# Optimization experiments

Measured on AMD Instinct MI355X. Metric: run time of the kernel, lower is better.

## Reference

```python
import jax, jax.numpy as jnp
import numpy as np

B, T, C = 8, 2048, 1024
HS = 64           # head_size
H = C // HS       # n_head = 16
LORA_R = 32       # per-branch lora rank (A is C x 32*5)
TD_R = 64         # time-decay lora rank


def setup_inputs() -> dict:
    key = jax.random.key(0)
    ks = jax.random.split(key, 20)
    inp = {
        "x": jax.random.normal(ks[0], (B, T, C), jnp.float32),
        "miu_x": jax.random.uniform(ks[1], (1, 1, C), jnp.float32),
        "lambda_": jax.random.uniform(ks[2], (5, 1, 1, C), jnp.float32),
        "A_lora": jax.random.normal(ks[3], (C, LORA_R * 5), jnp.float32) * 0.01,
        "B_lora": jax.random.normal(ks[4], (5, LORA_R, C), jnp.float32) * 0.01,
        "td_miu": -6.0 + 5.0 * jax.random.uniform(ks[5], (1, 1, C), jnp.float32),
        "td_A": jax.random.normal(ks[6], (C, TD_R), jnp.float32) * 0.01,
        "td_B": jax.random.normal(ks[7], (TD_R, C), jnp.float32) * 0.01,
        "u": jax.random.normal(ks[8], (H, HS), jnp.float32) * 0.1,
        "Wr": jax.random.normal(ks[9], (C, C), jnp.float32) * 0.02,
        "Wk": jax.random.normal(ks[10], (C, C), jnp.float32) * 0.02,
        "Wv": jax.random.normal(ks[11], (C, C), jnp.float32) * 0.02,
        "Wg": jax.random.normal(ks[12], (C, C), jnp.float32) * 0.02,
        "Wo": jax.random.normal(ks[13], (C, C), jnp.float32) * 0.02,
        "gn_gamma": jnp.ones((C,), jnp.float32),
        "gn_beta": jnp.zeros((C,), jnp.float32),
    }
    return inp


def _wkv6(r, k, v, w, u):
    """RWKV-6 selective-decay linear attention scan.
    r,k,v,w: (b, h, t, n); u: (h, n). Returns y: (b, h, t, n).
    State update: S = diag(exp(-exp(w_t))) S + k_t^T v_t;
    output: y_t = r_t @ (S + diag-free bonus u*k_t^T v_t)."""
    n = r.shape[-1]
    decay = jnp.exp(-jnp.exp(w))  # (b,h,t,n)

    def per_head(rt, kt, vt, dt, uh):  # (t,n) each, uh (n,)
        def step(S, inp):
            ri, ki, vi, di = inp
            kv = ki[:, None] * vi[None, :]          # (n,n)
            y = ri @ (S + uh[:, None] * kv)          # (n,)
            S = di[:, None] * S + kv
            return S, y
        S0 = jnp.zeros((n, n), rt.dtype)
        _, ys = jax.lax.scan(step, S0, (rt, kt, vt, dt))
        return ys  # (t,n)

    f = jax.vmap(per_head, in_axes=(0, 0, 0, 0, 0))       # heads
    f = jax.vmap(f, in_axes=(0, 0, 0, 0, None))           # batch
    return f(r, k, v, decay, u)


def reference(x, miu_x, lambda_, A_lora, B_lora, td_miu, td_A, td_B, u,
              Wr, Wk, Wv, Wg, Wo, gn_gamma, gn_beta):
    b, t, c = x.shape
    h, n = u.shape

    # time_shift: ZeroPad2d((0,0,1,-1)) -> previous token, zeros at t=0
    x_last = jnp.pad(x, ((0, 0), (1, 0), (0, 0)))[:, :t]
    dxa = x_last - x

    # ddlerp: lerp with static miu_x, then data-dependent LoRA mixing coeffs
    xm = x + dxa * miu_x  # (b,t,c)
    lora_h = jnp.tanh(xm @ A_lora).reshape(b, t, 5, -1)        # (b,t,5,32)
    miu = lambda_ + jnp.einsum('btfi,fic->fbtc', lora_h, B_lora)  # (5,b,t,c)
    xx = x[None] + dxa[None] * miu                             # (5,b,t,c)
    w_in, k_in, v_in, r_in, g_in = xx

    k = k_in @ Wk.T
    v = v_in @ Wv.T
    r = r_in @ Wr.T
    g = jax.nn.silu(g_in @ Wg.T)
    w = td_miu + jnp.tanh(w_in @ td_A) @ td_B  # (b,t,c)

    def to_heads(z):
        return z.reshape(b, t, h, n).transpose(0, 2, 1, 3)  # (b,h,t,n)

    y = _wkv6(to_heads(r), to_heads(k), to_heads(v), to_heads(w), u)
    y = y.transpose(0, 2, 1, 3)  # (b,t,h,n)

    # GroupNorm(n_head groups over C) per token, eps = 1e-5 * n_head
    eps = 1e-5 * h
    mean = y.mean(-1, keepdims=True)
    var = y.var(-1, keepdims=True)
    yn = (y - mean) * jax.lax.rsqrt(var + eps)
    yn = yn * gn_gamma.reshape(h, n) + gn_beta.reshape(h, n)
    yn = yn.reshape(b, t, c)

    return (yn * g) @ Wo.T
```

## Files before the change

### kernel.cpp

```cpp
#include <hip/hip_runtime.h>
#include <hip/hip_bf16.h>
#include <cstdint>

typedef __bf16 bf16_t;
typedef __bf16 bf16x8 __attribute__((ext_vector_type(8)));
typedef float f32x4 __attribute__((ext_vector_type(4)));

#define BB 8
#define TT 2048
#define TC 512
#define TCLOG 9
#define NCHUNK 4
#define MCH (BB*TC)
#define CCH 1024
#define HH 16
#define HSZ 64
#define LR5 160
#define LRP 192
#define TDR 64
#define TDK 128
#define TSUB 64
#define NSC (TC/TSUB)
#define BBHH (BB*HH)
#define LDP 72

#define BM 128
#define BN 128
#define BKK 64

enum { EPI_NONE = 0, EPI_SILU = 1, EPI_TANH = 2, EPI_XX = 3, EPI_WBIAS = 4 };

__device__ __forceinline__ void gload16(const bf16_t* g, bf16_t* l) {
    __builtin_amdgcn_global_load_lds(
        (__attribute__((address_space(1))) void*)(g),
        (__attribute__((address_space(3))) void*)(l), 16, 0, 0);
}

__global__ __launch_bounds__(256) void f2b_kernel(const float* __restrict__ in,
        bf16_t* __restrict__ out, int n) {
    int i = blockIdx.x * 256 + threadIdx.x;
    if (i < n) out[i] = (bf16_t)in[i];
}

__global__ __launch_bounds__(256) void transb_pad(const float* __restrict__ in,
        bf16_t* __restrict__ out, int R, int Cc, int Cp) {
    int i = blockIdx.x * 256 + threadIdx.x;
    if (i >= Cp * R) return;
    int row = i / R, col = i - row * R;
    out[i] = (row < Cc) ? (bf16_t)in[(size_t)col * Cc + row] : (bf16_t)0.f;
}

__global__ __launch_bounds__(256) void bbig_pad(const float* __restrict__ B_lora,
        bf16_t* __restrict__ Bbig) {
    int i = blockIdx.x * 256 + threadIdx.x;
    if (i >= 5 * CCH * LRP) return;
    int row = i / LRP, col = i - row * LRP;
    int f = row >> 10, c = row & (CCH - 1);
    int lo = f * 32;
    float v = 0.f;
    if (col >= lo && col < lo + 32)
        v = B_lora[(size_t)(lo + (col - lo)) * CCH + c];
    Bbig[i] = (bf16_t)v;
}

__global__ __launch_bounds__(256) void tdb2_kernel(const float* __restrict__ td_B,
        bf16_t* __restrict__ tdB2) {
    int i = blockIdx.x * 256 + threadIdx.x;
    if (i >= CCH * TDR) return;
    int n = i >> 6, k = i & 63;
    float f = td_B[(size_t)k * CCH + n];
    bf16_t hi = (bf16_t)f;
    bf16_t lo = (bf16_t)(f - (float)hi);
    tdB2[(size_t)n * TDK + k] = hi;
    tdB2[(size_t)n * TDK + TDR + k] = lo;
}

__global__ __launch_bounds__(256) void xm_kernel(const float* __restrict__ x,
        const float* __restrict__ miu_x, bf16_t* __restrict__ xm, int cOff) {
    long long i = (long long)blockIdx.x * 256 + threadIdx.x;
    int ch = (int)(i & (CCH - 1));
    int btl = (int)(i >> 10);
    int b = btl >> TCLOG, tau = btl & (TC - 1);
    int t = cOff + tau;
    size_t gi = ((size_t)b * TT + t) * CCH + ch;
    float xv = x[gi];
    float xp = (t > 0) ? x[gi - CCH] : 0.f;
    xm[i] = (bf16_t)(xv + (xp - xv) * miu_x[ch]);
}

struct GJob {
    const bf16_t* A;
    const bf16_t* Bw;
    void* C;
    int N;
    int nbmax;
    int K;
    int ldc;
    int epi;
    int outf32;
    int cmap;
    int dup;
};
struct GJobs { GJob j[5]; };

__global__ __launch_bounds__(256) void gemm_jobs(GJobs jobs,
        const float* __restrict__ x, const float* __restrict__ lam,
        const float* __restrict__ tdmiu, bf16_t* __restrict__ xx5, int cOff) {
    const GJob jb = jobs.j[blockIdx.z];
    const int n0 = blockIdx.y * BN;
    if (n0 >= jb.nbmax) return;
    const int m0 = blockIdx.x * BM;
    const int K = jb.K;
    __shared__ __align__(16) bf16_t As[BM * BKK];
    __shared__ __align__(16) bf16_t Bs[BN * BKK];
    const int tid = threadIdx.x;
    const int w = tid >> 6, lane = tid & 63;
    const int wm = (w >> 1) * 64, wn = (w & 1) * 64;
    const int lrow = lane & 15;
    const int kq = (lane >> 4) * 8;
    const int srow = tid >> 3;
    const int sc8 = (tid & 7) * 8;
    const bf16_t* Ab = jb.A + (size_t)m0 * K;
    const bf16_t* Bb = jb.Bw + (size_t)n0 * K;
    f32x4 acc[4][4] = {};
    for (int k0 = 0; k0 < K; k0 += BKK) {
        __syncthreads();
        #pragma unroll
        for (int p = 0; p < 4; ++p) {
            int r = srow + p * 32;
            gload16(Ab + (size_t)r * K + k0 + sc8, &As[(tid + p * 256) * 8]);
            gload16(Bb + (size_t)r * K + k0 + sc8, &Bs[(tid + p * 256) * 8]);
        }
        __syncthreads();
        #pragma unroll
        for (int kk = 0; kk < BKK; kk += 32) {
            bf16x8 af[4], bfr[4];
            #pragma unroll
            for (int mt = 0; mt < 4; ++mt)
                af[mt] = *(const bf16x8*)(&As[(wm + mt * 16 + lrow) * BKK + kk + kq]);
            #pragma unroll
            for (int nt = 0; nt < 4; ++nt)
                bfr[nt] = *(const bf16x8*)(&Bs[(wn + nt * 16 + lrow) * BKK + kk + kq]);
            #pragma unroll
            for (int mt = 0; mt < 4; ++mt)
                #pragma unroll
                for (int nt = 0; nt < 4; ++nt)
                    acc[mt][nt] = __builtin_amdgcn_mfma_f32_16x16x32_bf16(
                        af[mt], bfr[nt], acc[mt][nt], 0, 0, 0);
        }
    }
    const int rbase = (lane >> 4) * 4;
    const int col = lane & 15;
    if (jb.epi == EPI_XX) {
        #pragma unroll
        for (int mt = 0; mt < 4; ++mt)
            #pragma unroll
            for (int nt = 0; nt < 4; ++nt) {
                int n = n0 + wn + nt * 16 + col;
                int f = n >> 10, cch = n & (CCH - 1);
                #pragma unroll
                for (int rg = 0; rg < 4; ++rg) {
                    int m = m0 + wm + mt * 16 + rbase + rg;
                    int b = m >> TCLOG, tau = m & (TC - 1);
                    int t = cOff + tau;
                    size_t gi = ((size_t)b * TT + t) * CCH + cch;
                    float xv = x[gi];
                    float xp = (t > 0) ? x[gi - CCH] : 0.f;
                    float miu = lam[f * CCH + cch] + acc[mt][nt][rg];
                    xx5[(size_t)(f * MCH + m) * CCH + cch] =
                        (bf16_t)(xv + (xp - xv) * miu);
                }
            }
        return;
    }
    #pragma unroll
    for (int mt = 0; mt < 4; ++mt) {
        #pragma unroll
        for (int nt = 0; nt < 4; ++nt) {
            int n = n0 + wn + nt * 16 + col;
            if (n >= jb.N) continue;
            #pragma unroll
            for (int rg = 0; rg < 4; ++rg) {
                int m = m0 + wm + mt * 16 + rbase + rg;
                size_t mg = jb.cmap ? ((size_t)(m >> TCLOG) * TT + cOff + (m & (TC - 1)))
                                    : (size_t)m;
                float vv = acc[mt][nt][rg];
                if (jb.epi == EPI_SILU) vv = vv / (1.f + expf(-vv));
                else if (jb.epi == EPI_TANH) vv = tanhf(vv);
                else if (jb.epi == EPI_WBIAS) vv += tdmiu[n];
                if (jb.outf32) {
                    ((float*)jb.C)[mg * jb.ldc + n] = vv;
                } else {
                    bf16_t hv = (bf16_t)vv;
                    ((bf16_t*)jb.C)[mg * jb.ldc + n] = hv;
                    if (jb.dup) ((bf16_t*)jb.C)[mg * jb.ldc + n + TDR] = hv;
                }
            }
        }
    }
}

__global__ __launch_bounds__(64) void wkv_prepsg(const bf16_t* __restrict__ ry,
        const bf16_t* __restrict__ k, const float* __restrict__ w,
        const bf16_t* __restrict__ v, const float* __restrict__ u,
        bf16_t* __restrict__ rrT, bf16_t* __restrict__ ktT,
        float* __restrict__ PL, float* __restrict__ bvec,
        float* __restrict__ Sloc) {
    const int bh = blockIdx.x, sc = blockIdx.y;
    const int b = bh >> 4, h = bh & 15;
    const int j = threadIdx.x;
    const size_t base = ((size_t)b * TC + sc * TSUB) * CCH + h * HSZ + j;
    const size_t tile = ((size_t)bh * NSC + sc) * (TSUB * HSZ);
    const size_t vb = (size_t)bh * NSC + sc;
    __shared__ __align__(16) bf16_t ksT[HSZ * LDP];
    __shared__ __align__(16) bf16_t vtT[HSZ * LDP];
    __shared__ float pls[HSZ];
    const float uj = u[h * HSZ + j];
    float pex = 1.f;
    for (int t = 0; t < TSUB; ++t) {
        size_t idx = base + (size_t)t * CCH;
        float rv = (float)ry[idx], kv = (float)k[idx], wv = w[idx];
        bf16_t vv = v[idx];
        float d = expf(-expf(wv));
        rrT[tile + t * HSZ + j] = (bf16_t)(rv * pex);
        float pinc = pex * d;
        bf16_t ktv = (bf16_t)(kv / pinc);
        ktT[tile + t * HSZ + j] = ktv;
        ksT[j * LDP + t] = ktv;
        vtT[j * LDP + t] = vv;
        float bu = rv * uj * kv;
        #pragma unroll
        for (int off = 1; off < 64; off <<= 1) bu += __shfl_xor(bu, off);
        if (j == 0) bvec[vb * TSUB + t] = bu;
        pex = pinc;
    }
    PL[vb * HSZ + j] = pex;
    pls[j] = pex;
    __syncthreads();
    const int lrow = j & 15, kq = (j >> 4) * 8;
    f32x4 acc[4][4] = {};
    #pragma unroll
    for (int kk = 0; kk < TSUB; kk += 32) {
        bf16x8 af[4], bfr[4];
        #pragma unroll
        for (int mt = 0; mt < 4; ++mt)
            af[mt] = *(const bf16x8*)(&ksT[(mt * 16 + lrow) * LDP + kk + kq]);
        #pragma unroll
        for (int nt = 0; nt < 4; ++nt)
            bfr[nt] = *(const bf16x8*)(&vtT[(nt * 16 + lrow) * LDP + kk + kq]);
        #pragma unroll
        for (int mt = 0; mt < 4; ++mt)
            #pragma unroll
            for (int nt = 0; nt < 4; ++nt)
                acc[mt][nt] = __builtin_amdgcn_mfma_f32_16x16x32_bf16(
                    af[mt], bfr[nt], acc[mt][nt], 0, 0, 0);
    }
    const int rbase = (j >> 4) * 4, col = j & 15;
    #pragma unroll
    for (int mt = 0; mt < 4; ++mt)
        #pragma unroll
        for (int nt = 0; nt < 4; ++nt)
            #pragma unroll
            for (int rg = 0; rg < 4; ++rg) {
                int i = mt * 16 + rbase + rg, n = nt * 16 + col;
                Sloc[tile + i * HSZ + n] = pls[i] * acc[mt][nt][rg];
            }
}

__global__ __launch_bounds__(64) void wkv_combine(const float* __restrict__ Sloc,
        const float* __restrict__ PL, float* __restrict__ S0st,
        float* state, int cOuter) {
    const int bh = blockIdx.x;
    const int j = threadIdx.x;
    float* st = state + (size_t)bh * HSZ * HSZ;
    float S[HSZ];
    if (cOuter > 0) {
        #pragma unroll
        for (int i = 0; i < HSZ; ++i) S[i] = st[i * HSZ + j];
    } else {
        #pragma unroll
        for (int i = 0; i < HSZ; ++i) S[i] = 0.f;
    }
    __shared__ float pls[HSZ];
    for (int sc = 0; sc < NSC; ++sc) {
        const size_t so = ((size_t)bh * NSC + sc) * (HSZ * HSZ);
        pls[j] = PL[((size_t)bh * NSC + sc) * HSZ + j];
        __syncthreads();
        #pragma unroll
        for (int i = 0; i < HSZ; ++i) {
            S0st[so + i * HSZ + j] = S[i];
            S[i] = pls[i] * S[i] + Sloc[so + i * HSZ + j];
        }
        __syncthreads();
    }
    #pragma unroll
    for (int i = 0; i < HSZ; ++i) st[i * HSZ + j] = S[i];
}

__global__ __launch_bounds__(64) void wkv_y(bf16_t* __restrict__ ry,
        const bf16_t* __restrict__ rrT, const bf16_t* __restrict__ ktT,
        const bf16_t* __restrict__ v, const float* __restrict__ S0st,
        const float* __restrict__ bvec) {
    const int bh = blockIdx.x, sc = blockIdx.y;
    const int b = bh >> 4, h = bh & 15;
    const int j = threadIdx.x;
    const size_t tile = ((size_t)bh * NSC + sc) * (TSUB * HSZ);
    const size_t basev = ((size_t)b * TC + sc * TSUB) * CCH + h * HSZ;
    __shared__ __align__(16) bf16_t vtT[HSZ * LDP];
    __shared__ __align__(16) bf16_t s0T[HSZ * LDP];
    __shared__ __align__(16) bf16_t am[TSUB * LDP];
    __shared__ float bl[TSUB];
    for (int s = 0; s < TSUB; ++s)
        vtT[j * LDP + s] = v[basev + (size_t)s * CCH + j];
    for (int i = 0; i < HSZ; ++i)
        s0T[j * LDP + i] = (bf16_t)S0st[tile + i * HSZ + j];
    bl[j] = bvec[((size_t)bh * NSC + sc) * TSUB + j];
    __syncthreads();
    const bf16_t* rrt = rrT + tile;
    const bf16_t* ktt = ktT + tile;
    const int lane = j;
    const int lrow = lane & 15, kq = (lane >> 4) * 8;
    const int rbase = (lane >> 4) * 4, col = lane & 15;
    f32x4 acc[4][4] = {};
    #pragma unroll
    for (int kk = 0; kk < HSZ; kk += 32) {
        bf16x8 af[4], bfr[4];
        #pragma unroll
        for (int mt = 0; mt < 4; ++mt)
            af[mt] = *(const bf16x8*)(rrt + (mt * 16 + lrow) * HSZ + kk + kq);
        #pragma unroll
        for (int nt = 0; nt < 4; ++nt)
            bfr[nt] = *(const bf16x8*)(ktt + (nt * 16 + lrow) * HSZ + kk + kq);
        #pragma unroll
        for (int mt = 0; mt < 4; ++mt)
            #pragma unroll
            for (int nt = 0; nt < 4; ++nt)
                acc[mt][nt] = __builtin_amdgcn_mfma_f32_16x16x32_bf16(
                    af[mt], bfr[nt], acc[mt][nt], 0, 0, 0);
    }
    #pragma unroll
    for (int mt = 0; mt < 4; ++mt)
        #pragma unroll
        for (int nt = 0; nt < 4; ++nt)
            #pragma unroll
            for (int rg = 0; rg < 4; ++rg) {
                int t = mt * 16 + rbase + rg, s = nt * 16 + col;
                float aval = (s < t) ? acc[mt][nt][rg] : ((s == t) ? bl[t] : 0.f);
                am[t * LDP + s] = (bf16_t)aval;
            }
    __syncthreads();
    f32x4 yac[4][4] = {};
    #pragma unroll
    for (int kk = 0; kk < TSUB; kk += 32) {
        bf16x8 af[4], bfr[4];
        #pragma unroll
        for (int mt = 0; mt < 4; ++mt)
            af[mt] = *(const bf16x8*)(&am[(mt * 16 + lrow) * LDP + kk + kq]);
        #pragma unroll
        for (int nt = 0; nt < 4; ++nt)
            bfr[nt] = *(const bf16x8*)(&vtT[(nt * 16 + lrow) * LDP + kk + kq]);
        #pragma unroll
        for (int mt = 0; mt < 4; ++mt)
            #pragma unroll
            for (int nt = 0; nt < 4; ++nt)
                yac[mt][nt] = __builtin_amdgcn_mfma_f32_16x16x32_bf16(
                    af[mt], bfr[nt], yac[mt][nt], 0, 0, 0);
    }
    #pragma unroll
    for (int kk = 0; kk < HSZ; kk += 32) {
        bf16x8 af[4], bfr[4];
        #pragma unroll
        for (int mt = 0; mt < 4; ++mt)
            af[mt] = *(const bf16x8*)(rrt + (mt * 16 + lrow) * HSZ + kk + kq);
        #pragma unroll
        for (int nt = 0; nt < 4; ++nt)
            bfr[nt] = *(const bf16x8*)(&s0T[(nt * 16 + lrow) * LDP + kk + kq]);
        #pragma unroll
        for (int mt = 0; mt < 4; ++mt)
            #pragma unroll
            for (int nt = 0; nt < 4; ++nt)
                yac[mt][nt] = __builtin_amdgcn_mfma_f32_16x16x32_bf16(
                    af[mt], bfr[nt], yac[mt][nt], 0, 0, 0);
    }
    #pragma unroll
    for (int mt = 0; mt < 4; ++mt)
        #pragma unroll
        for (int nt = 0; nt < 4; ++nt)
            #pragma unroll
            for (int rg = 0; rg < 4; ++rg) {
                int t = mt * 16 + rbase + rg, jc = nt * 16 + col;
                ry[basev + (size_t)t * CCH + jc] = (bf16_t)yac[mt][nt][rg];
            }
}

__global__ __launch_bounds__(256) void gn_kernel(bf16_t* yg,
        const float* __restrict__ g_glob, const float* __restrict__ gamma,
        const float* __restrict__ beta, int cOff) {
    int wave = threadIdx.x >> 6, lane = threadIdx.x & 63;
    int gid = blockIdx.x * 4 + wave;
    int h = gid & (HH - 1);
    int ml = gid >> 4;
    int b = ml >> TCLOG, tau = ml & (TC - 1);
    size_t lidx = (size_t)ml * CCH + h * HSZ + lane;
    size_t gidx = ((size_t)b * TT + cOff + tau) * CCH + h * HSZ + lane;
    float val = (float)yg[lidx];
    float s = val, s2 = val * val;
    #pragma unroll
    for (int off = 32; off > 0; off >>= 1) {
        s  += __shfl_xor(s, off);
        s2 += __shfl_xor(s2, off);
    }
    float mean = s * (1.f / HSZ);
    float var  = fmaxf(s2 * (1.f / HSZ) - mean * mean, 0.f);
    float inv  = rsqrtf(var + 1e-5f * HH);
    float yn = (val - mean) * inv * gamma[h * HSZ + lane] + beta[h * HSZ + lane];
    yg[lidx] = (bf16_t)(yn * g_glob[gidx]);
}

extern "C" void kernel_launch(void* const* d_in, const int* in_sizes, int n_in,
                              void* d_out, int out_size, void* d_ws, size_t ws_size,
                              hipStream_t stream) {
    const float* x       = (const float*)d_in[0];
    const float* miu_x   = (const float*)d_in[1];
    const float* lambda_ = (const float*)d_in[2];
    const float* A_lora  = (const float*)d_in[3];
    const float* B_lora  = (const float*)d_in[4];
    const float* td_miu  = (const float*)d_in[5];
    const float* td_A    = (const float*)d_in[6];
    const float* td_B    = (const float*)d_in[7];
    const float* u       = (const float*)d_in[8];
    const float* Wr      = (const float*)d_in[9];
    const float* Wk      = (const float*)d_in[10];
    const float* Wv      = (const float*)d_in[11];
    const float* Wg      = (const float*)d_in[12];
    const float* Wo      = (const float*)d_in[13];
    const float* gamma   = (const float*)d_in[14];
    const float* beta    = (const float*)d_in[15];
    float* out = (float*)d_out;

    char* ws = (char*)d_ws;
    size_t off = 0;
    auto alloc = [&](size_t bytes) {
        char* p = ws + off;
        off += (bytes + 255) & ~(size_t)255;
        return (void*)p;
    };
    const size_t MCC = (size_t)MCH * CCH;
    bf16_t* xx5  = (bf16_t*)alloc(5 * MCC * 2);
    float*  Sloc = (float*)xx5;
    float*  S0st = (float*)(xx5 + 2 * MCC);
    bf16_t* xmb  = xx5 + 4 * MCC;
    bf16_t* kc   = (bf16_t*)alloc(MCC * 2);
    bf16_t* vc   = (bf16_t*)alloc(MCC * 2);
    float*  wc   = (float*)alloc(MCC * 4);
    bf16_t* ryc  = (bf16_t*)alloc(MCC * 2);
    bf16_t* rrT  = (bf16_t*)alloc(MCC * 2);
    bf16_t* ktT  = (bf16_t*)alloc(MCC * 2);
    bf16_t* lhcp = (bf16_t*)alloc((size_t)MCH * LRP * 2);
    bf16_t* tdh2 = (bf16_t*)alloc((size_t)MCH * TDK * 2);
    bf16_t* At   = (bf16_t*)alloc((size_t)256 * CCH * 2);
    bf16_t* tdAt = (bf16_t*)alloc((size_t)128 * CCH * 2);
    bf16_t* tdB2 = (bf16_t*)alloc((size_t)CCH * TDK * 2);
    bf16_t* Bbig = (bf16_t*)alloc((size_t)5 * CCH * LRP * 2);
    bf16_t* Wb[5];
    for (int i = 0; i < 5; ++i) Wb[i] = (bf16_t*)alloc((size_t)CCH * CCH * 2);
    float*  state = (float*)alloc((size_t)BBHH * HSZ * HSZ * 4);
    float*  PL    = (float*)alloc((size_t)BBHH * NSC * HSZ * 4);
    float*  bvec  = (float*)alloc((size_t)BBHH * NSC * TSUB * 4);
    (void)ws_size; (void)in_sizes; (void)n_in; (void)out_size;
    bf16_t* Wrb = Wb[0]; bf16_t* Wkb = Wb[1]; bf16_t* Wvb = Wb[2];
    bf16_t* Wgb = Wb[3]; bf16_t* Wob = Wb[4];

    const int WN = CCH * CCH;
    f2b_kernel<<<(WN + 255) / 256, 256, 0, stream>>>(Wr, Wrb, WN);
    f2b_kernel<<<(WN + 255) / 256, 256, 0, stream>>>(Wk, Wkb, WN);
    f2b_kernel<<<(WN + 255) / 256, 256, 0, stream>>>(Wv, Wvb, WN);
    f2b_kernel<<<(WN + 255) / 256, 256, 0, stream>>>(Wg, Wgb, WN);
    f2b_kernel<<<(WN + 255) / 256, 256, 0, stream>>>(Wo, Wob, WN);
    transb_pad<<<(256 * CCH + 255) / 256, 256, 0, stream>>>(A_lora, At, CCH, LR5, 256);
    transb_pad<<<(128 * CCH + 255) / 256, 256, 0, stream>>>(td_A, tdAt, CCH, TDR, 128);
    tdb2_kernel<<<(CCH * TDR + 255) / 256, 256, 0, stream>>>(td_B, tdB2);
    bbig_pad<<<(5 * CCH * LRP + 255) / 256, 256, 0, stream>>>(B_lora, Bbig);

    for (int c = 0; c < NCHUNK; ++c) {
        const int cOff = c * TC;
        xm_kernel<<<MCC / 256, 256, 0, stream>>>(x, miu_x, xmb, cOff);
        {
            GJobs J = {};
            J.j[0] = {xmb, At, lhcp, LRP, 256, CCH, LRP, EPI_TANH, 0, 0, 0};
            gemm_jobs<<<dim3(32, 2, 1), 256, 0, stream>>>(J, x, lambda_, td_miu, xx5, cOff);
        }
        {
            GJobs J = {};
            J.j[0] = {lhcp, Bbig, nullptr, 5 * CCH, 5 * CCH, LRP, 0, EPI_XX, 0, 0, 0};
            gemm_jobs<<<dim3(32, 40, 1), 256, 0, stream>>>(J, x, lambda_, td_miu, xx5, cOff);
        }
        {
            GJobs J = {};
            J.j[0] = {xx5 + 1 * MCC, Wkb,  kc,   CCH, CCH, CCH, CCH, EPI_NONE, 0, 0, 0};
            J.j[1] = {xx5 + 2 * MCC, Wvb,  vc,   CCH, CCH, CCH, CCH, EPI_NONE, 0, 0, 0};
            J.j[2] = {xx5 + 3 * MCC, Wrb,  ryc,  CCH, CCH, CCH, CCH, EPI_NONE, 0, 0, 0};
            J.j[3] = {xx5 + 4 * MCC, Wgb,  out,  CCH, CCH, CCH, CCH, EPI_SILU, 1, 1, 0};
            J.j[4] = {xx5 + 0 * MCC, tdAt, tdh2, TDR, 128, CCH, TDK, EPI_TANH, 0, 0, 1};
            gemm_jobs<<<dim3(32, 8, 5), 256, 0, stream>>>(J, x, lambda_, td_miu, xx5, cOff);
        }
        {
            GJobs J = {};
            J.j[0] = {tdh2, tdB2, wc, CCH, CCH, TDK, CCH, EPI_WBIAS, 1, 0, 0};
            gemm_jobs<<<dim3(32, 8, 1), 256, 0, stream>>>(J, x, lambda_, td_miu, xx5, cOff);
        }
        wkv_prepsg<<<dim3(BBHH, NSC), 64, 0, stream>>>(ryc, kc, wc, vc, u,
                                                       rrT, ktT, PL, bvec, Sloc);
        wkv_combine<<<BBHH, 64, 0, stream>>>(Sloc, PL, S0st, state, c);
        wkv_y<<<dim3(BBHH, NSC), 64, 0, stream>>>(ryc, rrT, ktT, vc, S0st, bvec);
        gn_kernel<<<(MCH * HH) / 4, 256, 0, stream>>>(ryc, out, gamma, beta, cOff);
        {
            GJobs J = {};
            J.j[0] = {ryc, Wob, out, CCH, CCH, CCH, CCH, EPI_NONE, 1, 1, 0};
            gemm_jobs<<<dim3(32, 8, 1), 256, 0, stream>>>(J, x, lambda_, td_miu, xx5, cOff);
        }
    }
}
```

Measured before the change: 1.464 ms.

## Precompute bf16 x and dx for EPI_XX epilogue and swizzle block order

The xm kernel now also writes bf16 copies of x and the token-shift delta into scratch buffers that alias kc/vc. The EPI_XX epilogue reads these two compact bf16 values per element instead of two fp32 loads from x with index math. Block indices are also remapped with an 8-way interleave, and the XX GEMM grid is transposed to be n-major, to change L2 reuse patterns. This rounds x and dx to bf16 before the lerp, which loses some precision. It also relies on kc/vc not being live until the next GEMM overwrites them.

```diff
diff --git a/kernel.cpp b/kernel.cpp
--- a/kernel.cpp
+++ b/kernel.cpp
@@ -76,7 +76,8 @@
 }
 
 __global__ __launch_bounds__(256) void xm_kernel(const float* __restrict__ x,
-        const float* __restrict__ miu_x, bf16_t* __restrict__ xm, int cOff) {
+        const float* __restrict__ miu_x, bf16_t* __restrict__ xm,
+        bf16_t* __restrict__ xb, bf16_t* __restrict__ dxb, int cOff) {
     long long i = (long long)blockIdx.x * 256 + threadIdx.x;
     int ch = (int)(i & (CCH - 1));
     int btl = (int)(i >> 10);
@@ -85,7 +86,10 @@
     size_t gi = ((size_t)b * TT + t) * CCH + ch;
     float xv = x[gi];
     float xp = (t > 0) ? x[gi - CCH] : 0.f;
-    xm[i] = (bf16_t)(xv + (xp - xv) * miu_x[ch]);
+    float dx = xp - xv;
+    xm[i]  = (bf16_t)(xv + dx * miu_x[ch]);
+    xb[i]  = (bf16_t)xv;
+    dxb[i] = (bf16_t)dx;
 }
 
 struct GJob {
@@ -104,12 +108,19 @@
 struct GJobs { GJob j[5]; };
 
 __global__ __launch_bounds__(256) void gemm_jobs(GJobs jobs,
-        const float* __restrict__ x, const float* __restrict__ lam,
-        const float* __restrict__ tdmiu, bf16_t* __restrict__ xx5, int cOff) {
+        const float* __restrict__ lam, const float* __restrict__ tdmiu,
+        const bf16_t* __restrict__ xb, const bf16_t* __restrict__ dxb,
+        bf16_t* __restrict__ xx5, int cOff) {
     const GJob jb = jobs.j[blockIdx.z];
-    const int n0 = blockIdx.y * BN;
+    const int nbx = gridDim.x;
+    int flat = blockIdx.y * nbx + blockIdx.x;
+    const int cpx = (nbx * gridDim.y) >> 3;
+    flat = (flat & 7) * cpx + (flat >> 3);
+    const int bx = flat % nbx, by = flat / nbx;
+    int m0, n0;
+    if (jb.epi == EPI_XX) { n0 = bx * BN; m0 = by * BM; }
+    else                  { m0 = bx * BM; n0 = by * BN; }
     if (n0 >= jb.nbmax) return;
-    const int m0 = blockIdx.x * BM;
     const int K = jb.K;
     __shared__ __align__(16) bf16_t As[BM * BKK];
     __shared__ __align__(16) bf16_t Bs[BN * BKK];
@@ -161,14 +172,11 @@
                 #pragma unroll
                 for (int rg = 0; rg < 4; ++rg) {
                     int m = m0 + wm + mt * 16 + rbase + rg;
-                    int b = m >> TCLOG, tau = m & (TC - 1);
-                    int t = cOff + tau;
-                    size_t gi = ((size_t)b * TT + t) * CCH + cch;
-                    float xv = x[gi];
-                    float xp = (t > 0) ? x[gi - CCH] : 0.f;
+                    size_t li = (size_t)m * CCH + cch;
+                    float xv = (float)xb[li];
+                    float dx = (float)dxb[li];
                     float miu = lam[f * CCH + cch] + acc[mt][nt][rg];
-                    xx5[(size_t)(f * MCH + m) * CCH + cch] =
-                        (bf16_t)(xv + (xp - xv) * miu);
+                    xx5[(size_t)(f * MCH + m) * CCH + cch] = (bf16_t)(xv + dx * miu);
                 }
             }
         return;
@@ -452,6 +460,8 @@
     bf16_t* xmb  = xx5 + 4 * MCC;
     bf16_t* kc   = (bf16_t*)alloc(MCC * 2);
     bf16_t* vc   = (bf16_t*)alloc(MCC * 2);
+    bf16_t* xb16 = kc;
+    bf16_t* dx16 = vc;
     float*  wc   = (float*)alloc(MCC * 4);
     bf16_t* ryc  = (bf16_t*)alloc(MCC * 2);
     bf16_t* rrT  = (bf16_t*)alloc(MCC * 2);
@@ -484,16 +494,16 @@
 
     for (int c = 0; c < NCHUNK; ++c) {
         const int cOff = c * TC;
-        xm_kernel<<<MCC / 256, 256, 0, stream>>>(x, miu_x, xmb, cOff);
+        xm_kernel<<<MCC / 256, 256, 0, stream>>>(x, miu_x, xmb, xb16, dx16, cOff);
         {
             GJobs J = {};
             J.j[0] = {xmb, At, lhcp, LRP, 256, CCH, LRP, EPI_TANH, 0, 0, 0};
-            gemm_jobs<<<dim3(32, 2, 1), 256, 0, stream>>>(J, x, lambda_, td_miu, xx5, cOff);
+            gemm_jobs<<<dim3(32, 2, 1), 256, 0, stream>>>(J, lambda_, td_miu, xb16, dx16, xx5, cOff);
         }
         {
             GJobs J = {};
             J.j[0] = {lhcp, Bbig, nullptr, 5 * CCH, 5 * CCH, LRP, 0, EPI_XX, 0, 0, 0};
-            gemm_jobs<<<dim3(32, 40, 1), 256, 0, stream>>>(J, x, lambda_, td_miu, xx5, cOff);
+            gemm_jobs<<<dim3(40, 32, 1), 256, 0, stream>>>(J, lambda_, td_miu, xb16, dx16, xx5, cOff);
         }
         {
             GJobs J = {};
@@ -502,12 +512,12 @@
             J.j[2] = {xx5 + 3 * MCC, Wrb,  ryc,  CCH, CCH, CCH, CCH, EPI_NONE, 0, 0, 0};
             J.j[3] = {xx5 + 4 * MCC, Wgb,  out,  CCH, CCH, CCH, CCH, EPI_SILU, 1, 1, 0};
             J.j[4] = {xx5 + 0 * MCC, tdAt, tdh2, TDR, 128, CCH, TDK, EPI_TANH, 0, 0, 1};
-            gemm_jobs<<<dim3(32, 8, 5), 256, 0, stream>>>(J, x, lambda_, td_miu, xx5, cOff);
+            gemm_jobs<<<dim3(32, 8, 5), 256, 0, stream>>>(J, lambda_, td_miu, xb16, dx16, xx5, cOff);
         }
         {
             GJobs J = {};
             J.j[0] = {tdh2, tdB2, wc, CCH, CCH, TDK, CCH, EPI_WBIAS, 1, 0, 0};
-            gemm_jobs<<<dim3(32, 8, 1), 256, 0, stream>>>(J, x, lambda_, td_miu, xx5, cOff);
+            gemm_jobs<<<dim3(32, 8, 1), 256, 0, stream>>>(J, lambda_, td_miu, xb16, dx16, xx5, cOff);
         }
         wkv_prepsg<<<dim3(BBHH, NSC), 64, 0, stream>>>(ryc, kc, wc, vc, u,
                                                        rrT, ktT, PL, bvec, Sloc);
@@ -517,7 +527,7 @@
         {
             GJobs J = {};
             J.j[0] = {ryc, Wob, out, CCH, CCH, CCH, CCH, EPI_NONE, 1, 1, 0};
-            gemm_jobs<<<dim3(32, 8, 1), 256, 0, stream>>>(J, x, lambda_, td_miu, xx5, cOff);
-        }
-    }
-}
+            gemm_jobs<<<dim3(32, 8, 1), 256, 0, stream>>>(J, lambda_, td_miu, xb16, dx16, xx5, cOff);
+        }
+    }
+}
```

Result: faster. 1.399 ms (-4.4%).
